# Performance work log

Hardware: AMD Instinct MI355X
Metric: run time of the kernel (lower is better)

## Reference

```python
import jax, jax.numpy as jnp
import numpy as np

B, L, H, C = 32, 2048, 512, 50
KERNEL = 3  # avgpool kernel, stride 1, pad 1, count_include_pad=False


def _avgpool3_no_pad_count(x):
    """AvgPool1d(kernel=3, stride=1, pad=1, count_include_pad=False) along last axis.
    x: (..., L). Zero-pad, sum 3-tap windows, divide by number of valid elements."""
    pad = [(0, 0)] * (x.ndim - 1) + [(1, 1)]
    xp = jnp.pad(x, pad)
    s = xp[..., :-2] + xp[..., 1:-1] + xp[..., 2:]
    ones = jnp.pad(jnp.ones_like(x), pad)
    cnt = ones[..., :-2] + ones[..., 1:-1] + ones[..., 2:]
    return s / cnt


def setup_inputs() -> dict:
    key = jax.random.key(0)
    k1, k2, k3, k4, k5, k6 = jax.random.split(key, 6)
    sent_keys = jax.random.normal(k1, (B, L, H), dtype=jnp.float32)
    sent_values = jax.random.normal(k2, (B, L, H), dtype=jnp.float32)
    sent_lens = jax.random.randint(k3, (B,), 1, L + 1).astype(jnp.int64)
    W1 = jax.random.normal(k4, (H, H), dtype=jnp.float32) * 0.02
    W2 = jax.random.normal(k5, (H, H), dtype=jnp.float32) * 0.02
    W3 = jax.random.normal(k6, (C, H), dtype=jnp.float32) * 0.02
    return {"sent_keys": sent_keys, "sent_values": sent_values,
            "sent_lens": sent_lens, "W1": W1, "W2": W2, "W3": W3}


def reference(sent_keys, sent_values, sent_lens, W1, W2, W3):
    # Tiny MLP scorer (dropout is identity in eval mode)
    p1 = jnp.tanh(jnp.einsum('blh,kh->blk', sent_keys, W1))   # (B,L,H)
    p2 = jnp.tanh(jnp.einsum('blh,kh->blk', p1, W2))          # (B,L,H)
    p3 = jnp.einsum('blh,ch->blc', p1 + p2, W3)               # (B,L,C)

    b, l, c = p3.shape
    # Fill padded positions with the score at the last valid position (index len-1)
    last_idx = (sent_lens - 1).astype(jnp.int32)[:, None, None]        # (B,1,1)
    last = jnp.take_along_axis(p3, jnp.broadcast_to(last_idx, (b, 1, c)), axis=1)  # (B,1,C)
    mask = (jnp.arange(l)[None, :] < sent_lens[:, None])[:, :, None]   # (B,L,1)
    kq = jnp.where(mask, p3, last)

    # Smooth along doc-position axis with avgpool(count_include_pad=False)
    smoothened_kq = _avgpool3_no_pad_count(kq.transpose(0, 2, 1)).transpose(0, 2, 1)  # (B,L,C)

    # Softmax over classes, then zero out padded positions
    attention_values = jax.nn.softmax(smoothened_kq, axis=2)
    attention_values = jnp.where(mask, attention_values, 0.0)

    # (B,C,L) @ (B,L,H) -> (B,C,H)
    class_inputs = jnp.einsum('blc,blh->bch', attention_values, sent_values)
    return attention_values, class_inputs, smoothened_kq
```

## Files before the change

### kernel.cpp

```cpp
#include <hip/hip_runtime.h>
#include <cstdint>

#define Bc 32
#define Lc 2048
#define Hc 512
#define Cc 50
#define PCc 52
#define Mc (Bc*Lc)

typedef short s8v   __attribute__((ext_vector_type(8)));
typedef float f4v   __attribute__((ext_vector_type(4)));

__device__ inline unsigned short f2bf(float f) {
    unsigned int u = __float_as_uint(f);
    u += 0x7fffu + ((u >> 16) & 1u);
    return (unsigned short)(u >> 16);
}
__device__ inline float bf2f(unsigned short h) {
    return __uint_as_float(((unsigned int)h) << 16);
}
__device__ inline float fast_tanh(float x) {
    float e = __expf(2.0f * x);
    return 1.0f - 2.0f / (e + 1.0f);
}
__device__ inline void gl_lds16(const unsigned short* g, unsigned short* l) {
    __builtin_amdgcn_global_load_lds(
        (const __attribute__((address_space(1))) unsigned int*)g,
        (__attribute__((address_space(3))) unsigned int*)l, 16, 0, 0);
}

__global__ __launch_bounds__(256)
void f32_to_bf16_kernel(const float* __restrict__ in, unsigned short* __restrict__ out)
{
    size_t i = ((size_t)blockIdx.x * 256 + threadIdx.x) * 8;
    float4 a = *(const float4*)(in + i);
    float4 b = *(const float4*)(in + i + 4);
    s8v o;
    o[0]=f2bf(a.x); o[1]=f2bf(a.y); o[2]=f2bf(a.z); o[3]=f2bf(a.w);
    o[4]=f2bf(b.x); o[5]=f2bf(b.y); o[6]=f2bf(b.z); o[7]=f2bf(b.w);
    *(s8v*)(out + i) = o;
}

__global__ __launch_bounds__(256)
void convert_weights_kernel(const float* __restrict__ W1, const float* __restrict__ W2,
                            const float* __restrict__ W3,
                            unsigned short* __restrict__ W1b,
                            unsigned short* __restrict__ W2b,
                            unsigned short* __restrict__ W3b)
{
    int e = (blockIdx.x * 256 + threadIdx.x) * 8;
    if (e >= 524288) {
        int off = e - 524288;
        int row = off >> 9;
        s8v o;
        #pragma unroll
        for (int j = 0; j < 8; ++j)
            o[j] = (row < Cc) ? (short)f2bf(W3[off + j]) : (short)0;
        *(s8v*)(W3b + off) = o;
        return;
    }
    const float* src = (e < 262144) ? W1 : W2;
    unsigned short* dst = (e < 262144) ? W1b : W2b;
    int off = (e < 262144) ? e : e - 262144;
    float4 a = *(const float4*)(src + off);
    float4 b = *(const float4*)(src + off + 4);
    s8v o;
    o[0]=f2bf(a.x); o[1]=f2bf(a.y); o[2]=f2bf(a.z); o[3]=f2bf(a.w);
    o[4]=f2bf(b.x); o[5]=f2bf(b.y); o[6]=f2bf(b.z); o[7]=f2bf(b.w);
    *(s8v*)(dst + off) = o;
}

__global__ __launch_bounds__(256)
void transpose_v_kernel(const float* __restrict__ V, unsigned short* __restrict__ Vt)
{
    __shared__ float tile[64 * 65];
    const int l0 = blockIdx.x * 64;
    const int h0 = blockIdx.y * 64;
    const int b  = blockIdx.z;
    const int tid = threadIdx.x;
    const int li = tid >> 2;
    const int hq = (tid & 3) * 4;

    const float* src = V + ((size_t)(b * Lc + l0 + li)) * Hc + h0 + hq;
    #pragma unroll
    for (int j = 0; j < 4; ++j) {
        float4 v = *(const float4*)(src + 16 * j);
        float* d = &tile[li * 65 + hq + 16 * j];
        d[0] = v.x; d[1] = v.y; d[2] = v.z; d[3] = v.w;
    }
    __syncthreads();

    const int lane = tid & 63;
    const int w4   = tid >> 6;
    const int lpos = (lane & 15) * 4;
    #pragma unroll
    for (int i = 0; i < 4; ++i) {
        int hr = i * 16 + w4 * 4 + (lane >> 4);
        ushort4 o;
        o.x = f2bf(tile[(lpos + 0) * 65 + hr]);
        o.y = f2bf(tile[(lpos + 1) * 65 + hr]);
        o.z = f2bf(tile[(lpos + 2) * 65 + hr]);
        o.w = f2bf(tile[(lpos + 3) * 65 + hr]);
        *(ushort4*)(Vt + ((size_t)(b * Hc + h0 + hr)) * Lc + l0 + lpos) = o;
    }
}

__global__ __launch_bounds__(256)
void mfma_gemm512(const unsigned short* __restrict__ Ab,
                  const unsigned short* __restrict__ Wb,
                  unsigned short* __restrict__ Ob, int mode)
{
    __shared__ alignas(16) unsigned short As[128 * 32];
    __shared__ alignas(16) unsigned short Bs[128 * 32];
    __shared__ alignas(16) float Esf[32 * 133];
    const int tid = threadIdx.x;
    const int w = tid >> 6, l = tid & 63;

    const int bid = blockIdx.x;
    const int ixd = bid >> 3;
    const int y   = (bid & 7) * 64 + (ixd >> 2);
    const int x   = ixd & 3;
    const int j0 = x * 128;
    const int i0 = y * 128;

    const int sr  = w * 16 + (l >> 2);
    const int kg8 = (l & 3) * 8;
    const unsigned short* Ag0 = Ab + (size_t)(i0 + sr) * 512 + kg8;
    const unsigned short* Ag1 = Ag0 + (size_t)64 * 512;
    const unsigned short* Bg0 = Wb + (size_t)(j0 + sr) * 512 + kg8;
    const unsigned short* Bg1 = Bg0 + (size_t)64 * 512;
    unsigned short* Al0 = As + w * 512;
    unsigned short* Al1 = As + 2048 + w * 512;
    unsigned short* Bl0 = Bs + w * 512;
    unsigned short* Bl1 = Bs + 2048 + w * 512;

    const int wm = (w & 1) * 64, wn = (w >> 1) * 64;
    const int fr = l & 15;
    const int fq = (l >> 4) * 8;

    f4v acc[4][4];
    #pragma unroll
    for (int r = 0; r < 4; ++r)
        #pragma unroll
        for (int c = 0; c < 4; ++c) acc[r][c] = (f4v){0.f, 0.f, 0.f, 0.f};

    for (int k0 = 0; k0 < 512; k0 += 32) {
        gl_lds16(Ag0 + k0, Al0);
        gl_lds16(Ag1 + k0, Al1);
        gl_lds16(Bg0 + k0, Bl0);
        gl_lds16(Bg1 + k0, Bl1);
        __syncthreads();
        s8v af[4], bf[4];
        #pragma unroll
        for (int r = 0; r < 4; ++r)
            af[r] = *(const s8v*)&As[(wm + r * 16 + fr) * 32 + fq];
        #pragma unroll
        for (int c = 0; c < 4; ++c)
            bf[c] = *(const s8v*)&Bs[(wn + c * 16 + fr) * 32 + fq];
        #pragma unroll
        for (int r = 0; r < 4; ++r)
            #pragma unroll
            for (int c = 0; c < 4; ++c)
                acc[r][c] = __builtin_amdgcn_mfma_f32_16x16x32_bf16(
                    af[r], bf[c], acc[r][c], 0, 0, 0);
        __syncthreads();
    }

    #pragma unroll
    for (int h = 0; h < 4; ++h) {
        if (h) __syncthreads();
        if ((w & 1) == (h >> 1)) {
            const int rr = (h & 1) * 2;
            #pragma unroll
            for (int r = 0; r < 2; ++r)
                #pragma unroll
                for (int c = 0; c < 4; ++c)
                    #pragma unroll
                    for (int v = 0; v < 4; ++v) {
                        int row = r * 16 + (l >> 4) * 4 + v;
                        int col = wn + c * 16 + fr;
                        Esf[row * 133 + col] = fast_tanh(acc[rr + r][c][v]);
                    }
        }
        __syncthreads();
        #pragma unroll
        for (int t = 0; t < 4; ++t) {
            int chunk = t * 256 + tid;
            int row = chunk >> 5;
            int c4  = (chunk & 31) * 4;
            f4v val = *(const f4v*)&Esf[row * 133 + c4];
            size_t gr   = (size_t)(i0 + (h >> 1) * 64 + (h & 1) * 32 + row);
            size_t goff = gr * 512 + j0 + c4;
            ushort4 o;
            if (mode) {
                ushort4 a = *(const ushort4*)(Ab + goff);
                o.x = f2bf(val[0] + bf2f(a.x));
                o.y = f2bf(val[1] + bf2f(a.y));
                o.z = f2bf(val[2] + bf2f(a.z));
                o.w = f2bf(val[3] + bf2f(a.w));
            } else {
                o.x = f2bf(val[0]); o.y = f2bf(val[1]);
                o.z = f2bf(val[2]); o.w = f2bf(val[3]);
            }
            *(ushort4*)(Ob + goff) = o;
        }
    }
}

__global__ __launch_bounds__(256)
void mfma_gemm_p3(const unsigned short* __restrict__ Sb,
                  const unsigned short* __restrict__ W3b,
                  float* __restrict__ P3)
{
    __shared__ alignas(16) char smem[24576];
    const int tid = threadIdx.x;
    const int w = tid >> 6, l = tid & 63;
    const int i0 = blockIdx.x * 128;

    const int sr  = w * 16 + (l >> 2);
    const int kg8 = (l & 3) * 8;
    const unsigned short* Ag0 = Sb + (size_t)(i0 + sr) * 512 + kg8;
    const unsigned short* Ag1 = Ag0 + (size_t)64 * 512;
    const unsigned short* Bg  = W3b + (size_t)sr * 512 + kg8;

    const int wm = w * 32;
    const int fr = l & 15;
    const int fq = (l >> 4) * 8;

    f4v acc[2][4];
    #pragma unroll
    for (int r = 0; r < 2; ++r)
        #pragma unroll
        for (int c = 0; c < 4; ++c) acc[r][c] = (f4v){0.f, 0.f, 0.f, 0.f};

    auto STAGE = [&](int buf, int k0) {
        unsigned short* a = (unsigned short*)(smem + buf * 12288);
        unsigned short* b = (unsigned short*)(smem + 8192 + buf * 12288);
        gl_lds16(Ag0 + k0, a + w * 512);
        gl_lds16(Ag1 + k0, a + 2048 + w * 512);
        gl_lds16(Bg  + k0, b + w * 512);
    };
    auto COMPUTE = [&](int buf) {
        const unsigned short* a = (const unsigned short*)(smem + buf * 12288);
        const unsigned short* b = (const unsigned short*)(smem + 8192 + buf * 12288);
        s8v af[2], bv[4];
        #pragma unroll
        for (int r = 0; r < 2; ++r)
            af[r] = *(const s8v*)&a[(wm + r * 16 + fr) * 32 + fq];
        #pragma unroll
        for (int c = 0; c < 4; ++c)
            bv[c] = *(const s8v*)&b[(c * 16 + fr) * 32 + fq];
        #pragma unroll
        for (int r = 0; r < 2; ++r)
            #pragma unroll
            for (int c = 0; c < 4; ++c)
                acc[r][c] = __builtin_amdgcn_mfma_f32_16x16x32_bf16(
                    af[r], bv[c], acc[r][c], 0, 0, 0);
    };

    STAGE(0, 0);
    #pragma unroll
    for (int t = 0; t < 15; ++t) {
        STAGE((t + 1) & 1, (t + 1) * 32);
        asm volatile("s_waitcnt vmcnt(3)" ::: "memory");
        __builtin_amdgcn_s_barrier();
        COMPUTE(t & 1);
        asm volatile("s_waitcnt lgkmcnt(0)" ::: "memory");
        __builtin_amdgcn_s_barrier();
    }
    asm volatile("s_waitcnt vmcnt(0)" ::: "memory");
    __builtin_amdgcn_s_barrier();
    COMPUTE(1);

    #pragma unroll
    for (int r = 0; r < 2; ++r)
        #pragma unroll
        for (int v = 0; v < 4; ++v) {
            const int row = i0 + wm + r * 16 + (l >> 4) * 4 + v;
            #pragma unroll
            for (int c = 0; c < 4; ++c) {
                const int col = c * 16 + fr;
                if (col < Cc) P3[(size_t)row * PCc + col] = acc[r][c][v];
            }
        }
}

__global__ __launch_bounds__(64)
void normalize_lens_kernel(const int* __restrict__ raw, int* __restrict__ lens)
{
    __shared__ int is64;
    if (threadIdx.x == 0) {
        int orv = 0;
        for (int i = 1; i < 32; i += 2) orv |= raw[i];
        is64 = (orv == 0) ? 1 : 0;
    }
    __syncthreads();
    int b = threadIdx.x;
    if (b < Bc) lens[b] = is64 ? raw[2*b] : raw[b];
}

__global__ __launch_bounds__(256)
void pool_softmax_kernel(const float* __restrict__ P3, const int* __restrict__ lens,
                         float* __restrict__ out_attn, float* __restrict__ out_smooth,
                         unsigned short* __restrict__ attnT)
{
    const int idx = blockIdx.x * 256 + threadIdx.x;
    const int b = idx >> 11;
    const int l = idx & (Lc - 1);
    const int len = lens[b];
    const float* base = P3 + (size_t)b * Lc * PCc;

    const int  r0 = min(l, len - 1);
    const bool hm = (l > 0);
    const bool hp = (l < Lc - 1);
    const int  rm = hm ? min(l - 1, len - 1) : 0;
    const int  rp = hp ? min(l + 1, len - 1) : 0;
    const float rcnt = 1.f / (1.f + (hm ? 1.f : 0.f) + (hp ? 1.f : 0.f));

    float sm[PCc];
    const float* p0 = base + (size_t)r0 * PCc;
    #pragma unroll
    for (int q = 0; q < 13; ++q) {
        f4v v = *(const f4v*)(p0 + q * 4);
        sm[q*4+0] = v[0]; sm[q*4+1] = v[1]; sm[q*4+2] = v[2]; sm[q*4+3] = v[3];
    }
    if (hm) {
        const float* p = base + (size_t)rm * PCc;
        #pragma unroll
        for (int q = 0; q < 13; ++q) {
            f4v v = *(const f4v*)(p + q * 4);
            sm[q*4+0] += v[0]; sm[q*4+1] += v[1]; sm[q*4+2] += v[2]; sm[q*4+3] += v[3];
        }
    }
    if (hp) {
        const float* p = base + (size_t)rp * PCc;
        #pragma unroll
        for (int q = 0; q < 13; ++q) {
            f4v v = *(const f4v*)(p + q * 4);
            sm[q*4+0] += v[0]; sm[q*4+1] += v[1]; sm[q*4+2] += v[2]; sm[q*4+3] += v[3];
        }
    }

    float mx = -1e30f;
    #pragma unroll
    for (int c = 0; c < Cc; ++c) {
        sm[c] *= rcnt;
        mx = fmaxf(mx, sm[c]);
    }
    float* srow = out_smooth + (size_t)idx * Cc;
    #pragma unroll
    for (int q = 0; q < 25; ++q) {
        float2 v = make_float2(sm[q*2], sm[q*2+1]);
        *(float2*)(srow + q * 2) = v;
    }

    float sum = 0.f;
    #pragma unroll
    for (int c = 0; c < Cc; ++c) {
        float e = __expf(sm[c] - mx);
        sm[c] = e;
        sum += e;
    }
    const float inv = 1.f / sum;
    const bool valid = (l < len);
    const float scale = valid ? inv : 0.f;
    float* arow = out_attn + (size_t)idx * Cc;
    unsigned short* trow = attnT + (size_t)b * 64 * Lc + l;
    #pragma unroll
    for (int c = 0; c < Cc; ++c) sm[c] *= scale;
    #pragma unroll
    for (int q = 0; q < 25; ++q)
        *(float2*)(arow + q * 2) = make_float2(sm[q*2], sm[q*2+1]);
    #pragma unroll
    for (int c = 0; c < Cc; ++c)
        trow[(size_t)c * Lc] = f2bf(sm[c]);
}

__global__ __launch_bounds__(256)
void class_mfma_kernel(const unsigned short* __restrict__ attnT,
                       const unsigned short* __restrict__ Vt,
                       float* __restrict__ out_class)
{
    __shared__ alignas(16) unsigned short As[64 * 32];
    __shared__ alignas(16) unsigned short Bs[128 * 32];
    const int tid = threadIdx.x;
    const int w = tid >> 6, l = tid & 63;

    const int bid  = blockIdx.x;
    const int ixd  = bid >> 3;
    const int pair = (bid & 7) * 16 + (ixd >> 2);
    const int n0 = (ixd & 3) * 128;
    const int b  = pair >> 2;
    const int kb = (pair & 3) * 512;

    const int sr  = w * 16 + (l >> 2);
    const int kg8 = (l & 3) * 8;
    const unsigned short* Ag  = attnT + ((size_t)b * 64 + sr) * Lc + kg8;
    const unsigned short* Bg0 = Vt + ((size_t)(b * Hc + n0 + sr)) * Lc + kg8;
    const unsigned short* Bg1 = Bg0 + (size_t)64 * Lc;
    unsigned short* Al  = As + w * 512;
    unsigned short* Bl0 = Bs + w * 512;
    unsigned short* Bl1 = Bs + 2048 + w * 512;

    const int fr = l & 15;
    const int fq = (l >> 4) * 8;

    f4v acc[4][2];
    #pragma unroll
    for (int r = 0; r < 4; ++r)
        #pragma unroll
        for (int c = 0; c < 2; ++c) acc[r][c] = (f4v){0.f, 0.f, 0.f, 0.f};

    for (int k0 = kb; k0 < kb + 512; k0 += 32) {
        gl_lds16(Ag + k0, Al);
        gl_lds16(Bg0 + k0, Bl0);
        gl_lds16(Bg1 + k0, Bl1);
        __syncthreads();
        s8v af[4], bv[2];
        #pragma unroll
        for (int r = 0; r < 4; ++r)
            af[r] = *(const s8v*)&As[(r * 16 + fr) * 32 + fq];
        #pragma unroll
        for (int c = 0; c < 2; ++c)
            bv[c] = *(const s8v*)&Bs[(w * 32 + c * 16 + fr) * 32 + fq];
        #pragma unroll
        for (int r = 0; r < 4; ++r)
            #pragma unroll
            for (int c = 0; c < 2; ++c)
                acc[r][c] = __builtin_amdgcn_mfma_f32_16x16x32_bf16(
                    af[r], bv[c], acc[r][c], 0, 0, 0);
        __syncthreads();
    }

    #pragma unroll
    for (int r = 0; r < 4; ++r)
        #pragma unroll
        for (int v = 0; v < 4; ++v) {
            const int m = r * 16 + (l >> 4) * 4 + v;
            if (m < Cc) {
                #pragma unroll
                for (int c = 0; c < 2; ++c) {
                    const int h = n0 + w * 32 + c * 16 + fr;
                    atomicAdd(out_class + ((size_t)b * Cc + m) * Hc + h,
                              acc[r][c][v]);
                }
            }
        }
}

extern "C" void kernel_launch(void* const* d_in, const int* in_sizes, int n_in,
                              void* d_out, int out_size, void* d_ws, size_t ws_size,
                              hipStream_t stream)
{
    const float* keys     = (const float*)d_in[0];
    const float* vals     = (const float*)d_in[1];
    const int*   lens_raw = (const int*)d_in[2];
    const float* W1       = (const float*)d_in[3];
    const float* W2       = (const float*)d_in[4];
    const float* W3       = (const float*)d_in[5];

    char* ws = (char*)d_ws;
    const size_t MB = 1024 * 1024;
    unsigned short* Akv  = (unsigned short*)ws;
    float*          P3   = (float*)ws;
    unsigned short* P1b  = (unsigned short*)(ws + 64 * MB);
    unsigned short* Vt   = (unsigned short*)(ws + 64 * MB);
    unsigned short* Sb   = (unsigned short*)(ws + 128 * MB);
    unsigned short* W1b  = (unsigned short*)(ws + 192 * MB);
    unsigned short* W2b  = W1b + Hc * Hc;
    unsigned short* W3b  = W2b + Hc * Hc;
    unsigned short* attnT= (unsigned short*)(ws + 194 * MB);
    int*            lens = (int*)(ws + 202 * MB);

    float* out_attn   = (float*)d_out;
    float* out_class  = out_attn + (size_t)Bc * Lc * Cc;
    float* out_smooth = out_class + (size_t)Bc * Cc * Hc;

    hipMemsetAsync(out_class, 0, (size_t)Bc * Cc * Hc * sizeof(float), stream);

    f32_to_bf16_kernel<<<(Mc * Hc / 8) / 256, 256, 0, stream>>>(keys, Akv);
    convert_weights_kernel<<<272, 256, 0, stream>>>(W1, W2, W3, W1b, W2b, W3b);
    normalize_lens_kernel<<<1, 64, 0, stream>>>(lens_raw, lens);

    mfma_gemm512<<<2048, 256, 0, stream>>>(Akv, W1b, P1b, 0);
    mfma_gemm512<<<2048, 256, 0, stream>>>(P1b, W2b, Sb, 1);
    transpose_v_kernel<<<dim3(Lc / 64, Hc / 64, Bc), 256, 0, stream>>>(vals, Vt);
    mfma_gemm_p3<<<Mc / 128, 256, 0, stream>>>(Sb, W3b, P3);
    pool_softmax_kernel<<<Mc / 256, 256, 0, stream>>>(P3, lens, out_attn, out_smooth, attnT);
    class_mfma_kernel<<<512, 256, 0, stream>>>(attnT, Vt, out_class);
}
```

Baseline: 498.6 us.

## Fuse second MLP GEMM, residual add and W3 projection into one kernel

The second 512x512 GEMM (tanh, plus p1 residual) and the W3 class projection now run in a single kernel. Each 512-thread block computes a full 64-row by 512-column strip, adds tanh to the staged p1 rows in LDS, then runs the 50-class MFMA directly from shared memory. This removes the bf16 Sb intermediate round trip through global memory and one kernel launch. In exchange, every block re-streams all of W2 without double buffering. The large LDS footprint also limits occupancy, so the GEMM itself may run less efficiently than the tiled 128x128 version.

```diff
diff --git a/kernel.cpp b/kernel.cpp
--- a/kernel.cpp
+++ b/kernel.cpp
@@ -108,7 +108,7 @@
 __global__ __launch_bounds__(256)
 void mfma_gemm512(const unsigned short* __restrict__ Ab,
                   const unsigned short* __restrict__ Wb,
-                  unsigned short* __restrict__ Ob, int mode)
+                  unsigned short* __restrict__ Ob)
 {
     __shared__ alignas(16) unsigned short As[128 * 32];
     __shared__ alignas(16) unsigned short Bs[128 * 32];
@@ -192,96 +192,114 @@
             size_t gr   = (size_t)(i0 + (h >> 1) * 64 + (h & 1) * 32 + row);
             size_t goff = gr * 512 + j0 + c4;
             ushort4 o;
-            if (mode) {
-                ushort4 a = *(const ushort4*)(Ab + goff);
-                o.x = f2bf(val[0] + bf2f(a.x));
-                o.y = f2bf(val[1] + bf2f(a.y));
-                o.z = f2bf(val[2] + bf2f(a.z));
-                o.w = f2bf(val[3] + bf2f(a.w));
-            } else {
-                o.x = f2bf(val[0]); o.y = f2bf(val[1]);
-                o.z = f2bf(val[2]); o.w = f2bf(val[3]);
-            }
+            o.x = f2bf(val[0]); o.y = f2bf(val[1]);
+            o.z = f2bf(val[2]); o.w = f2bf(val[3]);
             *(ushort4*)(Ob + goff) = o;
         }
     }
 }
 
-__global__ __launch_bounds__(256)
-void mfma_gemm_p3(const unsigned short* __restrict__ Sb,
-                  const unsigned short* __restrict__ W3b,
-                  float* __restrict__ P3)
-{
-    __shared__ alignas(16) char smem[24576];
+__global__ __launch_bounds__(512, 4)
+void mfma_gemm2_fused(const unsigned short* __restrict__ Ab,
+                      const unsigned short* __restrict__ Wb,
+                      const unsigned short* __restrict__ W3g,
+                      float* __restrict__ P3)
+{
+    __shared__ alignas(16) char smem[66560];
+    unsigned short* Ast = (unsigned short*)smem;
+    unsigned short* Bst = (unsigned short*)(smem + 4096);
+    unsigned short* Ss  = (unsigned short*)smem;
+
     const int tid = threadIdx.x;
     const int w = tid >> 6, l = tid & 63;
-    const int i0 = blockIdx.x * 128;
-
-    const int sr  = w * 16 + (l >> 2);
-    const int kg8 = (l & 3) * 8;
-    const unsigned short* Ag0 = Sb + (size_t)(i0 + sr) * 512 + kg8;
-    const unsigned short* Ag1 = Ag0 + (size_t)64 * 512;
-    const unsigned short* Bg  = W3b + (size_t)sr * 512 + kg8;
-
-    const int wm = w * 32;
-    const int fr = l & 15;
-    const int fq = (l >> 4) * 8;
-
-    f4v acc[2][4];
-    #pragma unroll
-    for (int r = 0; r < 2; ++r)
+    const int i0 = blockIdx.x * 64;
+
+    const int sr  = tid >> 2;
+    const int kg8 = (tid & 3) * 8;
+    const int fr  = l & 15;
+    const int fq  = (l >> 4) * 8;
+    const int wn  = w * 64;
+
+    const unsigned short* AgP = Ab + (size_t)(i0 + sr) * 512 + kg8;
+    const unsigned short* BgP = Wb + (size_t)sr * 512 + kg8;
+
+    f4v acc[4][4];
+    #pragma unroll
+    for (int r = 0; r < 4; ++r)
         #pragma unroll
         for (int c = 0; c < 4; ++c) acc[r][c] = (f4v){0.f, 0.f, 0.f, 0.f};
 
-    auto STAGE = [&](int buf, int k0) {
-        unsigned short* a = (unsigned short*)(smem + buf * 12288);
-        unsigned short* b = (unsigned short*)(smem + 8192 + buf * 12288);
-        gl_lds16(Ag0 + k0, a + w * 512);
-        gl_lds16(Ag1 + k0, a + 2048 + w * 512);
-        gl_lds16(Bg  + k0, b + w * 512);
-    };
-    auto COMPUTE = [&](int buf) {
-        const unsigned short* a = (const unsigned short*)(smem + buf * 12288);
-        const unsigned short* b = (const unsigned short*)(smem + 8192 + buf * 12288);
-        s8v af[2], bv[4];
-        #pragma unroll
-        for (int r = 0; r < 2; ++r)
-            af[r] = *(const s8v*)&a[(wm + r * 16 + fr) * 32 + fq];
+    for (int k0 = 0; k0 < 512; k0 += 32) {
+        if (tid < 256)
+            gl_lds16(AgP + k0, Ast + sr * 32 + kg8);
+        #pragma unroll
+        for (int rr = 0; rr < 4; ++rr)
+            gl_lds16(BgP + (size_t)rr * 128 * 512 + k0,
+                     Bst + (rr * 128 + sr) * 32 + kg8);
+        __syncthreads();
+        s8v af[4], bv[4];
+        #pragma unroll
+        for (int r = 0; r < 4; ++r)
+            af[r] = *(const s8v*)&Ast[(r * 16 + fr) * 32 + fq];
         #pragma unroll
         for (int c = 0; c < 4; ++c)
-            bv[c] = *(const s8v*)&b[(c * 16 + fr) * 32 + fq];
-        #pragma unroll
-        for (int r = 0; r < 2; ++r)
+            bv[c] = *(const s8v*)&Bst[(wn + c * 16 + fr) * 32 + fq];
+        #pragma unroll
+        for (int r = 0; r < 4; ++r)
             #pragma unroll
             for (int c = 0; c < 4; ++c)
                 acc[r][c] = __builtin_amdgcn_mfma_f32_16x16x32_bf16(
                     af[r], bv[c], acc[r][c], 0, 0, 0);
-    };
-
-    STAGE(0, 0);
-    #pragma unroll
-    for (int t = 0; t < 15; ++t) {
-        STAGE((t + 1) & 1, (t + 1) * 32);
-        asm volatile("s_waitcnt vmcnt(3)" ::: "memory");
-        __builtin_amdgcn_s_barrier();
-        COMPUTE(t & 1);
-        asm volatile("s_waitcnt lgkmcnt(0)" ::: "memory");
-        __builtin_amdgcn_s_barrier();
-    }
-    asm volatile("s_waitcnt vmcnt(0)" ::: "memory");
-    __builtin_amdgcn_s_barrier();
-    COMPUTE(1);
-
+        __syncthreads();
+    }
+
+    {
+        const int row = tid >> 3;
+        const int c0  = (tid & 7) * 8;
+        #pragma unroll
+        for (int q = 0; q < 8; ++q) {
+            int col = c0 + q * 64;
+            *(s8v*)&Ss[row * 520 + col] =
+                *(const s8v*)(Ab + (size_t)(i0 + row) * 512 + col);
+        }
+    }
+    __syncthreads();
+
+    #pragma unroll
+    for (int r = 0; r < 4; ++r)
+        #pragma unroll
+        for (int c = 0; c < 4; ++c)
+            #pragma unroll
+            for (int v = 0; v < 4; ++v) {
+                int row = r * 16 + (l >> 4) * 4 + v;
+                int col = wn + c * 16 + fr;
+                unsigned short* p = &Ss[row * 520 + col];
+                *p = f2bf(bf2f(*p) + fast_tanh(acc[r][c][v]));
+            }
+    __syncthreads();
+
+    const int cb = (w & 3) * 16;
+    const int rh = (w >> 2) * 32;
+    f4v acc3[2];
+    acc3[0] = (f4v){0.f, 0.f, 0.f, 0.f};
+    acc3[1] = (f4v){0.f, 0.f, 0.f, 0.f};
+    #pragma unroll
+    for (int ks = 0; ks < 16; ++ks) {
+        s8v bv3 = *(const s8v*)(W3g + (size_t)(cb + fr) * 512 + ks * 32 + fq);
+        #pragma unroll
+        for (int r = 0; r < 2; ++r) {
+            s8v av = *(const s8v*)&Ss[(rh + r * 16 + fr) * 520 + ks * 32 + fq];
+            acc3[r] = __builtin_amdgcn_mfma_f32_16x16x32_bf16(
+                av, bv3, acc3[r], 0, 0, 0);
+        }
+    }
     #pragma unroll
     for (int r = 0; r < 2; ++r)
         #pragma unroll
         for (int v = 0; v < 4; ++v) {
-            const int row = i0 + wm + r * 16 + (l >> 4) * 4 + v;
-            #pragma unroll
-            for (int c = 0; c < 4; ++c) {
-                const int col = c * 16 + fr;
-                if (col < Cc) P3[(size_t)row * PCc + col] = acc[r][c][v];
-            }
+            const int row = i0 + rh + r * 16 + (l >> 4) * 4 + v;
+            const int cls = cb + fr;
+            if (cls < Cc) P3[(size_t)row * PCc + cls] = acc3[r][v];
         }
 }
 
@@ -465,7 +483,6 @@
     float*          P3   = (float*)ws;
     unsigned short* P1b  = (unsigned short*)(ws + 64 * MB);
     unsigned short* Vt   = (unsigned short*)(ws + 64 * MB);
-    unsigned short* Sb   = (unsigned short*)(ws + 128 * MB);
     unsigned short* W1b  = (unsigned short*)(ws + 192 * MB);
     unsigned short* W2b  = W1b + Hc * Hc;
     unsigned short* W3b  = W2b + Hc * Hc;
@@ -482,10 +499,9 @@
     convert_weights_kernel<<<272, 256, 0, stream>>>(W1, W2, W3, W1b, W2b, W3b);
     normalize_lens_kernel<<<1, 64, 0, stream>>>(lens_raw, lens);
 
-    mfma_gemm512<<<2048, 256, 0, stream>>>(Akv, W1b, P1b, 0);
-    mfma_gemm512<<<2048, 256, 0, stream>>>(P1b, W2b, Sb, 1);
+    mfma_gemm512<<<2048, 256, 0, stream>>>(Akv, W1b, P1b);
+    mfma_gemm2_fused<<<Mc / 64, 512, 0, stream>>>(P1b, W2b, W3b, P3);
     transpose_v_kernel<<<dim3(Lc / 64, Hc / 64, Bc), 256, 0, stream>>>(vals, Vt);
-    mfma_gemm_p3<<<Mc / 128, 256, 0, stream>>>(Sb, W3b, P3);
     pool_softmax_kernel<<<Mc / 256, 256, 0, stream>>>(P3, lens, out_attn, out_smooth, attnT);
     class_mfma_kernel<<<512, 256, 0, stream>>>(attnT, Vt, out_class);
 }
```

Result: faster. 477.5 us (-4.2%).
